# Kernel optimization log

Hardware: AMD Instinct MI355X
Metric: run time of the kernel (lower is better)

The kernel has to match this reference:

```python
import jax, jax.numpy as jnp
import numpy as np

B, N, HD = 4, 2048, 256
E, T = 4096, 1024
PROPAG_STEPS = 5
ALPHA_MAX = 0.2
LN_EPS = 1e-5


def setup_inputs() -> dict:
    key = jax.random.key(0)
    ks = jax.random.split(key, 16)
    s_in, s_h = (2.0 * HD) ** -0.5, HD ** -0.5
    return {
        "attr_matrix": jax.random.normal(ks[0], (B, N, 1), dtype=jnp.float32),
        "adj_matrix": jax.random.uniform(ks[1], (B, N, N), dtype=jnp.float32),
        # ggnn.linear_i: 1 -> HD
        "W_i": jax.random.normal(ks[2], (HD, 1), dtype=jnp.float32),
        "b_i": jnp.zeros((HD,), dtype=jnp.float32),
        # ggnn.gru: GRUCell(input=2*HD, hidden=HD), torch gate order r,z,n
        "W_ih": jax.random.normal(ks[3], (3 * HD, 2 * HD), dtype=jnp.float32) * s_in,
        "b_ih": jnp.zeros((3 * HD,), dtype=jnp.float32),
        "W_hh": jax.random.normal(ks[4], (3 * HD, HD), dtype=jnp.float32) * s_h,
        "b_hh": jnp.zeros((3 * HD,), dtype=jnp.float32),
        # ggnn.linear_o: HD -> 1
        "W_o": jax.random.normal(ks[5], (1, HD), dtype=jnp.float32) * s_h,
        "b_o": jnp.zeros((1,), dtype=jnp.float32),
        # topo buffers (incidence-like, kept small to mimic sparse +/-1 matrices)
        "B1": jax.random.normal(ks[6], (N, E), dtype=jnp.float32) * 0.02,
        "B2": jax.random.normal(ks[7], (E, T), dtype=jnp.float32) * 0.02,
        # topo trainables
        "proj_W": jax.random.normal(ks[8], (HD, HD), dtype=jnp.float32) * s_h,
        "ln_gamma": jnp.ones((HD,), dtype=jnp.float32),
        "ln_beta": jnp.zeros((HD,), dtype=jnp.float32),
        "alpha_raw": jnp.float32(-2.0),
    }


def _gru_cell(x, h, W_ih, b_ih, W_hh, b_hh):
    # x: [B,N,2H], h: [B,N,H]; torch GRUCell gate order: r, z, n
    gx = jnp.einsum('bni,gi->bng', x, W_ih) + b_ih
    gh = jnp.einsum('bnh,gh->bng', h, W_hh) + b_hh
    xr, xz, xn = jnp.split(gx, 3, axis=-1)
    hr, hz, hn = jnp.split(gh, 3, axis=-1)
    r = jax.nn.sigmoid(xr + hr)
    z = jax.nn.sigmoid(xz + hz)
    n = jnp.tanh(xn + r * hn)
    return (1.0 - z) * n + z * h


def _layernorm(x, gamma, beta):
    mu = jnp.mean(x, axis=-1, keepdims=True)
    var = jnp.mean(jnp.square(x - mu), axis=-1, keepdims=True)
    return (x - mu) * jax.lax.rsqrt(var + LN_EPS) * gamma + beta


def reference(attr_matrix, adj_matrix, W_i, b_i, W_ih, b_ih, W_hh, b_hh,
              W_o, b_o, B1, B2, proj_W, ln_gamma, ln_beta, alpha_raw):
    A_in = adj_matrix                      # [B,N,N]
    A_out = jnp.swapaxes(adj_matrix, -2, -1)
    # linear_i + relu
    h = jax.nn.relu(jnp.einsum('bnc,hc->bnh', attr_matrix, W_i) + b_i)  # [B,N,H]
    # GGNN propagation
    for _ in range(PROPAG_STEPS):
        a_in = jnp.einsum('bnm,bmh->bnh', A_in, h)
        a_out = jnp.einsum('bnm,bmh->bnh', A_out, h)
        h = _gru_cell(jnp.concatenate((a_in, a_out), axis=-1), h,
                      W_ih, b_ih, W_hh, b_hh)
    # topo residual: dH = B1 (L1 (B1^T h)), L1 = B1^T B1 + B2 B2^T
    L1 = B1.T @ B1 + B2 @ B2.T             # [E,E]
    E_feat = jnp.einsum('ne,bnh->beh', B1, h)       # B1^T H
    E_topo = jnp.einsum('ef,bfh->beh', L1, E_feat)
    dH = jnp.einsum('ne,beh->bnh', B1, E_topo)
    dH = _layernorm(jax.nn.relu(jnp.einsum('bnh,oh->bno', dH, proj_W)),
                    ln_gamma, ln_beta)
    alpha = ALPHA_MAX * jax.nn.sigmoid(alpha_raw)
    h = h + alpha * dH
    # linear_o -> [B,N] (squeeze(0) is a no-op for B>1)
    anomaly = (jnp.einsum('bnh,oh->bno', h, W_o) + b_o)[..., 0]
    return anomaly
```

## Files before the change

### kernel.cpp

```cpp
#include <hip/hip_runtime.h>
#include <hip/hip_fp16.h>


typedef __bf16 bf16x8 __attribute__((ext_vector_type(8)));
typedef _Float16 f16x8 __attribute__((ext_vector_type(8)));
typedef float f32x4 __attribute__((ext_vector_type(4)));

#define BM 128
#define BN 128
#define BK 16
#define LO_INV (1.f / 1024.f)

__device__ __forceinline__ unsigned short bf16rne(float x)
{
    unsigned u = __float_as_uint(x);
    return (unsigned short)((u + 0x7FFFu + ((u >> 16) & 1u)) >> 16);
}
__device__ __forceinline__ float bf2f(unsigned short h)
{
    return __uint_as_float((unsigned)h << 16);
}
__device__ __forceinline__ void split2(float x, unsigned short& hi, unsigned short& lo)
{
    hi = bf16rne(x);
    lo = bf16rne(x - bf2f(hi));
}

__device__ __forceinline__ unsigned short f16r(float x)
{
    return __half_as_ushort(__float2half(x));
}
__device__ __forceinline__ float f16f(unsigned short u)
{
    return __half2float(__ushort_as_half(u));
}
__device__ __forceinline__ void splitf(float x, unsigned short& hi, unsigned short& lo)
{
    hi = f16r(x);
    lo = f16r((x - f16f(hi)) * 1024.f);
}

__device__ __forceinline__ void gload_lds16(const unsigned short* g, unsigned short* l)
{
    __builtin_amdgcn_global_load_lds(
        (const __attribute__((address_space(1))) void*)g,
        (__attribute__((address_space(3))) void*)l, 16, 0, 0);
}

__device__ __forceinline__ void stage2(const unsigned short* g, unsigned short* l, int K)
{
    gload_lds16(g, l);
    gload_lds16(g + (size_t)32 * K, l + 2048);
}

template<int SPLIT>
__device__ __forceinline__ void mm_loop64f(
    const unsigned short* ag0, const unsigned short* ag1,
    const unsigned short* bg0, const unsigned short* bg1,
    int K, unsigned short* LDS, int tid,
    f32x4 (&acc0)[2][2], f32x4 (&acc1)[2][2])
{
    constexpr int NT = SPLIT ? 2 : 1;
    constexpr int TSZ = 4096;

    int lane = tid & 63, r16 = lane & 15, g = lane >> 4, s7 = r16 & 7;
    int wv = tid >> 6, wr = wv >> 1, wc = wv & 1;
    int arow = (wr * 32 + r16) * 128;
    int brow = (wc * 32 + r16) * 128;
    unsigned short* lA = LDS + (tid >> 6) * 512;
    unsigned short* lB = LDS + NT * TSZ + (tid >> 6) * 512;
    const char* Ab = (const char*)LDS;
    const char* Bb = (const char*)(LDS + NT * TSZ);

    for (int k0 = 0; k0 < K; k0 += 64) {
        stage2(ag0 + k0, lA, K);
        if constexpr (SPLIT) stage2(ag1 + k0, lA + TSZ, K);
        stage2(bg0 + k0, lB, K);
        if constexpr (SPLIT) stage2(bg1 + k0, lB + TSZ, K);
        __syncthreads();
#pragma unroll
        for (int ks = 0; ks < 2; ++ks) {
            int tt = ((ks * 4 + g) ^ s7) * 16;
            f16x8 a0[2], a1[2], b0[2], b1[2];
#pragma unroll
            for (int mi = 0; mi < 2; ++mi) {
                a0[mi] = *(const f16x8*)(Ab + arow + mi * 2048 + tt);
                if constexpr (SPLIT)
                    a1[mi] = *(const f16x8*)(Ab + TSZ * 2 + arow + mi * 2048 + tt);
            }
#pragma unroll
            for (int ni = 0; ni < 2; ++ni) {
                b0[ni] = *(const f16x8*)(Bb + brow + ni * 2048 + tt);
                if constexpr (SPLIT)
                    b1[ni] = *(const f16x8*)(Bb + TSZ * 2 + brow + ni * 2048 + tt);
            }
#pragma unroll
            for (int mi = 0; mi < 2; ++mi)
#pragma unroll
                for (int ni = 0; ni < 2; ++ni) {
                    if constexpr (SPLIT) {
                        acc1[mi][ni] = __builtin_amdgcn_mfma_f32_16x16x32_f16(
                            a1[mi], b0[ni], acc1[mi][ni], 0, 0, 0);
                        acc1[mi][ni] = __builtin_amdgcn_mfma_f32_16x16x32_f16(
                            a0[mi], b1[ni], acc1[mi][ni], 0, 0, 0);
                    }
                    acc0[mi][ni] = __builtin_amdgcn_mfma_f32_16x16x32_f16(
                        a0[mi], b0[ni], acc0[mi][ni], 0, 0, 0);
                }
        }
        __syncthreads();
    }
}

template<int SPLIT, int OF16>
__global__ __launch_bounds__(256, 2) void mm_f16(
    const unsigned short* __restrict__ Ah, const unsigned short* __restrict__ Al,
    const unsigned short* __restrict__ Bh, const unsigned short* __restrict__ Bl,
    int K, const float* __restrict__ bias, const float* __restrict__ Cacc,
    void* __restrict__ Cout, int ldc)
{
    constexpr int NT = SPLIT ? 2 : 1;
    __shared__ unsigned short LDS[2 * NT * 4096];
    int tid = threadIdx.x;

    unsigned nwg = gridDim.x * gridDim.y;
    unsigned lin = blockIdx.y * gridDim.x + blockIdx.x;
    unsigned wk = ((nwg & 7) == 0) ? (lin & 7) * (nwg >> 3) + (lin >> 3) : lin;
    unsigned bx = wk % gridDim.x, by = wk / gridDim.x;

    int m0 = by * 64, n0 = bx * 64;
    int rp = tid >> 3, sl8 = ((tid & 7) ^ (rp & 7)) * 8;
    const unsigned short* ag0 = Ah + (size_t)(m0 + rp) * K + sl8;
    const unsigned short* ag1 = SPLIT ? Al + (size_t)(m0 + rp) * K + sl8 : nullptr;
    const unsigned short* bg0 = Bh + (size_t)(n0 + rp) * K + sl8;
    const unsigned short* bg1 = SPLIT ? Bl + (size_t)(n0 + rp) * K + sl8 : nullptr;

    f32x4 acc0[2][2], acc1[2][2];
#pragma unroll
    for (int mi = 0; mi < 2; ++mi)
#pragma unroll
        for (int ni = 0; ni < 2; ++ni) {
            acc0[mi][ni] = (f32x4){0.f, 0.f, 0.f, 0.f};
            acc1[mi][ni] = (f32x4){0.f, 0.f, 0.f, 0.f};
        }

    mm_loop64f<SPLIT>(ag0, ag1, bg0, bg1, K, LDS, tid, acc0, acc1);

    int lane = tid & 63, r16 = lane & 15, g = lane >> 4;
    int wv = tid >> 6, wr = wv >> 1, wc = wv & 1;
#pragma unroll
    for (int mi = 0; mi < 2; ++mi) {
#pragma unroll
        for (int ni = 0; ni < 2; ++ni) {
            int col = n0 + wc * 32 + ni * 16 + r16;
            float badd = bias ? bias[col] : 0.f;
#pragma unroll
            for (int j = 0; j < 4; ++j) {
                int row = m0 + wr * 32 + mi * 16 + g * 4 + j;
                float v = acc0[mi][ni][j] + badd;
                if (SPLIT) v += acc1[mi][ni][j] * LO_INV;
                if (Cacc) v += Cacc[(size_t)row * ldc + col];
                if (OF16)
                    ((unsigned short*)Cout)[(size_t)row * ldc + col] = f16r(v);
                else
                    ((float*)Cout)[(size_t)row * ldc + col] = v;
            }
        }
    }
}

__global__ __launch_bounds__(256, 2) void gxgru(
    const unsigned short* __restrict__ Xhi, const unsigned short* __restrict__ Xlo,
    const unsigned short* __restrict__ WihH, const unsigned short* __restrict__ WihL,
    const float* __restrict__ b_ih, const float* __restrict__ ghb,
    float* __restrict__ h)
{
    __shared__ unsigned short LDS[32768];
    int tid = threadIdx.x;

    unsigned lin = blockIdx.y * 4 + blockIdx.x;
    unsigned wk = (lin & 7) * 64 + (lin >> 3);
    unsigned tb = wk & 3, by = wk >> 2;

    int m0 = by * 64;
    const int K = 512;
    int rp = tid >> 3, sl8 = ((tid & 7) ^ (rp & 7)) * 8;
    const unsigned short* ag0 = Xhi + (size_t)(m0 + rp) * K + sl8;
    const unsigned short* ag1 = Xlo + (size_t)(m0 + rp) * K + sl8;
    const unsigned short* bh0 = WihH + (size_t)(tb * 192 + rp) * K + sl8;
    const unsigned short* bl0 = WihL + (size_t)(tb * 192 + rp) * K + sl8;

    int lane = tid & 63, r16 = lane & 15, lg = lane >> 4, s7 = r16 & 7;
    int wv = tid >> 6, wr = wv >> 1, wc = wv & 1;
    int arow = (wr * 32 + r16) * 128;
    int brow = (wc * 32 + r16) * 128;
    unsigned short* lA = LDS + (tid >> 6) * 512;
    unsigned short* lB = LDS + 8192 + (tid >> 6) * 512;

    f32x4 acc0[3][2][2], acc1[3][2][2];
#pragma unroll
    for (int g = 0; g < 3; ++g)
#pragma unroll
        for (int mi = 0; mi < 2; ++mi)
#pragma unroll
            for (int ni = 0; ni < 2; ++ni) {
                acc0[g][mi][ni] = (f32x4){0.f, 0.f, 0.f, 0.f};
                acc1[g][mi][ni] = (f32x4){0.f, 0.f, 0.f, 0.f};
            }

    for (int k0 = 0; k0 < K; k0 += 64) {
        stage2(ag0 + k0, lA, K);
        stage2(ag1 + k0, lA + 4096, K);
#pragma unroll
        for (int g = 0; g < 3; ++g) {
            stage2(bh0 + (size_t)(g * 64) * K + k0, lB + g * 4096, K);
            stage2(bl0 + (size_t)(g * 64) * K + k0, lB + 12288 + g * 4096, K);
        }
        __syncthreads();
#pragma unroll
        for (int ks = 0; ks < 2; ++ks) {
            int tt = ((ks * 4 + lg) ^ s7) * 16;
            f16x8 a0[2], a1[2];
#pragma unroll
            for (int mi = 0; mi < 2; ++mi) {
                a0[mi] = *(const f16x8*)((const char*)LDS + arow + mi * 2048 + tt);
                a1[mi] = *(const f16x8*)((const char*)LDS + 8192 + arow + mi * 2048 + tt);
            }
#pragma unroll
            for (int g = 0; g < 3; ++g) {
                f16x8 b0[2], b1[2];
#pragma unroll
                for (int ni = 0; ni < 2; ++ni) {
                    b0[ni] = *(const f16x8*)((const char*)LDS + 16384 + g * 8192 +
                                             brow + ni * 2048 + tt);
                    b1[ni] = *(const f16x8*)((const char*)LDS + 40960 + g * 8192 +
                                             brow + ni * 2048 + tt);
                }
#pragma unroll
                for (int mi = 0; mi < 2; ++mi)
#pragma unroll
                    for (int ni = 0; ni < 2; ++ni) {
                        acc1[g][mi][ni] = __builtin_amdgcn_mfma_f32_16x16x32_f16(
                            a1[mi], b0[ni], acc1[g][mi][ni], 0, 0, 0);
                        acc1[g][mi][ni] = __builtin_amdgcn_mfma_f32_16x16x32_f16(
                            a0[mi], b1[ni], acc1[g][mi][ni], 0, 0, 0);
                        acc0[g][mi][ni] = __builtin_amdgcn_mfma_f32_16x16x32_f16(
                            a0[mi], b0[ni], acc0[g][mi][ni], 0, 0, 0);
                    }
            }
        }
        __syncthreads();
    }

#pragma unroll
    for (int mi = 0; mi < 2; ++mi) {
#pragma unroll
        for (int ni = 0; ni < 2; ++ni) {
            int t = tb * 64 + wc * 32 + ni * 16 + r16;
            float br = b_ih[t], bz = b_ih[256 + t], bn = b_ih[512 + t];
#pragma unroll
            for (int j = 0; j < 4; ++j) {
                int row = m0 + wr * 32 + mi * 16 + lg * 4 + j;
                float xr = acc0[0][mi][ni][j] + acc1[0][mi][ni][j] * LO_INV + br;
                float xz = acc0[1][mi][ni][j] + acc1[1][mi][ni][j] * LO_INV + bz;
                float xn = acc0[2][mi][ni][j] + acc1[2][mi][ni][j] * LO_INV + bn;
                size_t grow = (size_t)row * 768;
                float hr = ghb[grow + t];
                float hz = ghb[grow + 256 + t];
                float hn = ghb[grow + 512 + t];
                float r = 1.f / (1.f + __expf(-(xr + hr)));
                float z = 1.f / (1.f + __expf(-(xz + hz)));
                float nn = tanhf(xn + r * hn);
                size_t hix = (size_t)row * 256 + t;
                h[hix] = (1.f - z) * nn + z * h[hix];
            }
        }
    }
}

__global__ __launch_bounds__(256, 2) void mm_step1f(
    const unsigned short* __restrict__ AhHi, const unsigned short* __restrict__ AhLo,
    const unsigned short* __restrict__ AtHi, const unsigned short* __restrict__ AtLo,
    const unsigned short* __restrict__ hTh, const unsigned short* __restrict__ hTl,
    unsigned short* __restrict__ Xhi, unsigned short* __restrict__ Xlo,
    const unsigned short* __restrict__ hrmh, const unsigned short* __restrict__ hrml,
    const unsigned short* __restrict__ WhhH, const unsigned short* __restrict__ WhhL,
    const float* __restrict__ b_hh, float* __restrict__ ghb)
{
    __shared__ unsigned short LDS[16384];
    int tid = threadIdx.x;
    unsigned bid = blockIdx.x;
    int lane = tid & 63, r16 = lane & 15, g = lane >> 4;
    int wv = tid >> 6, wr = wv >> 1, wc = wv & 1;
    int rp = tid >> 3, sl8 = ((tid & 7) ^ (rp & 7)) * 8;

    f32x4 acc0[2][2], acc1[2][2];
#pragma unroll
    for (int mi = 0; mi < 2; ++mi)
#pragma unroll
        for (int ni = 0; ni < 2; ++ni) {
            acc0[mi][ni] = (f32x4){0.f, 0.f, 0.f, 0.f};
            acc1[mi][ni] = (f32x4){0.f, 0.f, 0.f, 0.f};
        }

    if (bid < 1024) {
        unsigned wk = (bid & 7) * 128 + (bid >> 3);
        unsigned bz = wk >> 7, rem = wk & 127, by = rem >> 2, bx = rem & 3;
        int b = bz >> 1, wio = bz & 1;
        const unsigned short* Ahp = (wio ? AtHi : AhHi) + (size_t)b * 4194304;
        const unsigned short* Alp = (wio ? AtLo : AhLo) + (size_t)b * 4194304;
        size_t boff = (size_t)(b * 256 + bx * 64) * 2048;
        int m0 = by * 64;
        const int K = 2048;
        const unsigned short* ag0 = Ahp + (size_t)(m0 + rp) * K + sl8;
        const unsigned short* ag1 = Alp + (size_t)(m0 + rp) * K + sl8;
        const unsigned short* bg0 = hTh + boff + (size_t)rp * K + sl8;
        const unsigned short* bg1 = hTl + boff + (size_t)rp * K + sl8;

        mm_loop64f<1>(ag0, ag1, bg0, bg1, K, LDS, tid, acc0, acc1);

        float* T = reinterpret_cast<float*>(LDS);
#pragma unroll
        for (int mi = 0; mi < 2; ++mi)
#pragma unroll
            for (int ni = 0; ni < 2; ++ni)
#pragma unroll
                for (int j = 0; j < 4; ++j)
                    T[(wr * 32 + mi * 16 + g * 4 + j) * 68 +
                      wc * 32 + ni * 16 + r16] =
                        acc0[mi][ni][j] + acc1[mi][ni][j] * LO_INV;
        __syncthreads();

        int row = tid >> 2, fq = tid & 3;
        const float* src = T + row * 68 + fq * 16;
        unsigned hw[8], lw[8];
#pragma unroll
        for (int e = 0; e < 8; ++e) {
            unsigned short h0, l0, h1, l1;
            splitf(src[2 * e], h0, l0);
            splitf(src[2 * e + 1], h1, l1);
            hw[e] = (unsigned)h0 | ((unsigned)h1 << 16);
            lw[e] = (unsigned)l0 | ((unsigned)l1 << 16);
        }
        size_t base = ((size_t)(m0 + row) * 4 + b) * 512 + wio * 256 + bx * 64 + fq * 16;
        ((uint4*)(Xhi + base))[0] = (uint4){hw[0], hw[1], hw[2], hw[3]};
        ((uint4*)(Xhi + base))[1] = (uint4){hw[4], hw[5], hw[6], hw[7]};
        ((uint4*)(Xlo + base))[0] = (uint4){lw[0], lw[1], lw[2], lw[3]};
        ((uint4*)(Xlo + base))[1] = (uint4){lw[4], lw[5], lw[6], lw[7]};
    } else {
        unsigned gidx = bid - 1024;
        unsigned by = gidx / 12, bx = gidx % 12;
        int m0 = by * 64, n0 = bx * 64;
        const int K = 256;
        const unsigned short* ag0 = hrmh + (size_t)(m0 + rp) * K + sl8;
        const unsigned short* ag1 = hrml + (size_t)(m0 + rp) * K + sl8;
        const unsigned short* bg0 = WhhH + (size_t)(n0 + rp) * K + sl8;
        const unsigned short* bg1 = WhhL + (size_t)(n0 + rp) * K + sl8;

        mm_loop64f<1>(ag0, ag1, bg0, bg1, K, LDS, tid, acc0, acc1);

#pragma unroll
        for (int mi = 0; mi < 2; ++mi) {
#pragma unroll
            for (int ni = 0; ni < 2; ++ni) {
                int col = n0 + wc * 32 + ni * 16 + r16;
                float badd = b_hh[col];
#pragma unroll
                for (int j = 0; j < 4; ++j) {
                    int row = m0 + wr * 32 + mi * 16 + g * 4 + j;
                    ghb[(size_t)row * 768 + col] =
                        acc0[mi][ni][j] + acc1[mi][ni][j] * LO_INV + badd;
                }
            }
        }
    }
}

__global__ void split_adj16(const float* __restrict__ adj,
                            unsigned short* __restrict__ nhi, unsigned short* __restrict__ nlo,
                            unsigned short* __restrict__ thi, unsigned short* __restrict__ tlo)
{
    __shared__ float t[64][68];
    int z = blockIdx.z;
    const float* src = adj + (size_t)z * 4194304;
    int tx = threadIdx.x & 15, ty = threadIdx.x >> 4;
    int i0 = blockIdx.y * 64, j0 = blockIdx.x * 64;
#pragma unroll
    for (int i = 0; i < 4; ++i) {
        int r = ty * 4 + i;
        float4 v = *(const float4*)(src + (size_t)(i0 + r) * 2048 + j0 + tx * 4);
        ushort4 h, l;
        splitf(v.x, h.x, l.x); splitf(v.y, h.y, l.y);
        splitf(v.z, h.z, l.z); splitf(v.w, h.w, l.w);
        size_t o = (size_t)z * 4194304 + (size_t)(i0 + r) * 2048 + j0 + tx * 4;
        *(ushort4*)(nhi + o) = h; *(ushort4*)(nlo + o) = l;
        t[r][tx * 4 + 0] = v.x; t[r][tx * 4 + 1] = v.y;
        t[r][tx * 4 + 2] = v.z; t[r][tx * 4 + 3] = v.w;
    }
    __syncthreads();
#pragma unroll
    for (int i = 0; i < 4; ++i) {
        int r = ty * 4 + i;
        ushort4 h, l;
        splitf(t[tx * 4 + 0][r], h.x, l.x);
        splitf(t[tx * 4 + 1][r], h.y, l.y);
        splitf(t[tx * 4 + 2][r], h.z, l.z);
        splitf(t[tx * 4 + 3][r], h.w, l.w);
        size_t o = (size_t)z * 4194304 + (size_t)(j0 + r) * 2048 + i0 + tx * 4;
        *(ushort4*)(thi + o) = h; *(ushort4*)(tlo + o) = l;
    }
}

__global__ void split_h16(const float* __restrict__ h,
                          unsigned short* __restrict__ hi, unsigned short* __restrict__ lo,
                          unsigned short* __restrict__ hrmh, unsigned short* __restrict__ hrml)
{
    __shared__ float t[64][68];
    int f0 = blockIdx.x * 64, n0 = blockIdx.y * 64;
    int tx = threadIdx.x & 15, ty = threadIdx.x >> 4;
#pragma unroll
    for (int i = 0; i < 4; ++i) {
        int r = ty * 4 + i;
        float4 v = *(const float4*)(h + (size_t)(n0 + r) * 1024 + f0 + tx * 4);
        t[r][tx * 4 + 0] = v.x; t[r][tx * 4 + 1] = v.y;
        t[r][tx * 4 + 2] = v.z; t[r][tx * 4 + 3] = v.w;
        if (hrmh) {
            ushort4 hh, ll;
            splitf(v.x, hh.x, ll.x); splitf(v.y, hh.y, ll.y);
            splitf(v.z, hh.z, ll.z); splitf(v.w, hh.w, ll.w);
            size_t o = (size_t)(n0 + r) * 1024 + f0 + tx * 4;
            *(ushort4*)(hrmh + o) = hh;
            *(ushort4*)(hrml + o) = ll;
        }
    }
    __syncthreads();
#pragma unroll
    for (int i = 0; i < 4; ++i) {
        int r = ty * 4 + i;
        ushort4 hh, ll;
        splitf(t[tx * 4 + 0][r], hh.x, ll.x);
        splitf(t[tx * 4 + 1][r], hh.y, ll.y);
        splitf(t[tx * 4 + 2][r], hh.z, ll.z);
        splitf(t[tx * 4 + 3][r], hh.w, ll.w);
        size_t o = (size_t)(f0 + r) * 2048 + n0 + tx * 4;
        *(ushort4*)(hi + o) = hh; *(ushort4*)(lo + o) = ll;
    }
}

__global__ void split_t16(const float* __restrict__ in, unsigned short* __restrict__ outN,
                          unsigned short* __restrict__ outT, int R, int C)
{
    __shared__ float t[64][68];
    int i0 = blockIdx.y * 64, j0 = blockIdx.x * 64;
    int tx = threadIdx.x & 15, ty = threadIdx.x >> 4;
#pragma unroll
    for (int i = 0; i < 4; ++i) {
        int r = ty * 4 + i;
        float4 v = *(const float4*)(in + (size_t)(i0 + r) * C + j0 + tx * 4);
        ushort4 hh;
        hh.x = f16r(v.x); hh.y = f16r(v.y);
        hh.z = f16r(v.z); hh.w = f16r(v.w);
        *(ushort4*)(outN + (size_t)(i0 + r) * C + j0 + tx * 4) = hh;
        t[r][tx * 4 + 0] = v.x; t[r][tx * 4 + 1] = v.y;
        t[r][tx * 4 + 2] = v.z; t[r][tx * 4 + 3] = v.w;
    }
    __syncthreads();
#pragma unroll
    for (int i = 0; i < 4; ++i) {
        int r = ty * 4 + i;
        ushort4 hh;
        hh.x = f16r(t[tx * 4 + 0][r]);
        hh.y = f16r(t[tx * 4 + 1][r]);
        hh.z = f16r(t[tx * 4 + 2][r]);
        hh.w = f16r(t[tx * 4 + 3][r]);
        *(ushort4*)(outT + (size_t)(j0 + r) * R + i0 + tx * 4) = hh;
    }
}

__global__ void split_w16(const float* __restrict__ Wih, const float* __restrict__ Whh,
                          const float* __restrict__ pj,
                          unsigned short* __restrict__ WihH, unsigned short* __restrict__ WihL,
                          unsigned short* __restrict__ WhhH, unsigned short* __restrict__ WhhL,
                          unsigned short* __restrict__ pjH)
{
    int i = blockIdx.x * 256 + threadIdx.x;
    if (i < 393216) {
        int row = i >> 9, col = i & 511;
        int g = row >> 8, t = row & 255;
        int nrow = (t >> 6) * 192 + g * 64 + (t & 63);
        unsigned short h, l;
        splitf(Wih[i], h, l);
        WihH[nrow * 512 + col] = h; WihL[nrow * 512 + col] = l;
    } else if (i < 589824) {
        int j = i - 393216;
        unsigned short h, l;
        splitf(Whh[j], h, l);
        WhhH[j] = h; WhhL[j] = l;
    } else if (i < 655360) {
        int j = i - 589824;
        pjH[j] = f16r(pj[j]);
    }
}

__global__ __launch_bounds__(256, 2) void gemm_f32(
    const float* __restrict__ A, const float* __restrict__ B, float* __restrict__ C,
    int M, int N, int K, int lda, int ldb, int ldc,
    long sA, long sB, long sC,
    const float* __restrict__ bias, int ta, int tb, int accum)
{
    int bz = blockIdx.z;
    int taEff = ta;
    if (ta == 2) {
        int b = bz >> 1, w = bz & 1;
        A += (long)b * sA; B += (long)b * sB; C += (long)b * sC + w * 256;
        taEff = w;
    } else {
        A += (long)bz * sA; B += (long)bz * sB; C += (long)bz * sC;
    }
    int m0 = blockIdx.y * BM, n0 = blockIdx.x * BN;

    __shared__ float As[BK][BM + 4];
    __shared__ float Bs[BK][BN + 4];

    int tid = threadIdx.x;
    int tx = tid & 15, ty = tid >> 4;

    float acc[64];
#pragma unroll
    for (int i = 0; i < 64; ++i) acc[i] = 0.f;

    for (int k0 = 0; k0 < K; k0 += BK) {
        if (!taEff) {
            int m = tid >> 1, kk = (tid & 1) * 8;
            const float* src = A + (long)(m0 + m) * lda + (k0 + kk);
            float4 v0 = *(const float4*)(src);
            float4 v1 = *(const float4*)(src + 4);
            As[kk + 0][m] = v0.x; As[kk + 1][m] = v0.y;
            As[kk + 2][m] = v0.z; As[kk + 3][m] = v0.w;
            As[kk + 4][m] = v1.x; As[kk + 5][m] = v1.y;
            As[kk + 6][m] = v1.z; As[kk + 7][m] = v1.w;
        } else {
            int k = tid >> 4, mm = (tid & 15) * 8;
            const float* src = A + (long)(k0 + k) * lda + (m0 + mm);
            *(float4*)&As[k][mm]     = *(const float4*)(src);
            *(float4*)&As[k][mm + 4] = *(const float4*)(src + 4);
        }
        if (!tb) {
            int k = tid >> 4, nn = (tid & 15) * 8;
            const float* src = B + (long)(k0 + k) * ldb + (n0 + nn);
            *(float4*)&Bs[k][nn]     = *(const float4*)(src);
            *(float4*)&Bs[k][nn + 4] = *(const float4*)(src + 4);
        } else {
            int n = tid >> 1, kk = (tid & 1) * 8;
            const float* src = B + (long)(n0 + n) * ldb + (k0 + kk);
            float4 v0 = *(const float4*)(src);
            float4 v1 = *(const float4*)(src + 4);
            Bs[kk + 0][n] = v0.x; Bs[kk + 1][n] = v0.y;
            Bs[kk + 2][n] = v0.z; Bs[kk + 3][n] = v0.w;
            Bs[kk + 4][n] = v1.x; Bs[kk + 5][n] = v1.y;
            Bs[kk + 6][n] = v1.z; Bs[kk + 7][n] = v1.w;
        }
        __syncthreads();

#pragma unroll
        for (int k = 0; k < BK; ++k) {
            float a[8], b[8];
            *(float4*)&a[0] = *(const float4*)&As[k][ty * 4];
            *(float4*)&a[4] = *(const float4*)&As[k][64 + ty * 4];
            *(float4*)&b[0] = *(const float4*)&Bs[k][tx * 4];
            *(float4*)&b[4] = *(const float4*)&Bs[k][64 + tx * 4];
#pragma unroll
            for (int i = 0; i < 8; ++i)
#pragma unroll
                for (int j = 0; j < 8; ++j)
                    acc[i * 8 + j] += a[i] * b[j];
        }
        __syncthreads();
    }

#pragma unroll
    for (int i = 0; i < 8; ++i) {
        int row = m0 + ((i >> 2) ? 64 : 0) + ty * 4 + (i & 3);
#pragma unroll
        for (int jh = 0; jh < 2; ++jh) {
            int col = n0 + jh * 64 + tx * 4;
            float4 v;
            v.x = acc[i * 8 + jh * 4 + 0];
            v.y = acc[i * 8 + jh * 4 + 1];
            v.z = acc[i * 8 + jh * 4 + 2];
            v.w = acc[i * 8 + jh * 4 + 3];
            if (bias) {
                v.x += bias[col + 0]; v.y += bias[col + 1];
                v.z += bias[col + 2]; v.w += bias[col + 3];
            }
            float* dst = C + (long)row * ldc + col;
            if (accum) {
                float4 o = *(const float4*)dst;
                v.x += o.x; v.y += o.y; v.z += o.z; v.w += o.w;
            }
            *(float4*)dst = v;
        }
    }
}

__global__ void split_adj(const float* __restrict__ adj,
                          unsigned short* __restrict__ nhi, unsigned short* __restrict__ nlo,
                          unsigned short* __restrict__ thi, unsigned short* __restrict__ tlo)
{
    __shared__ float t[64][68];
    int z = blockIdx.z;
    const float* src = adj + (size_t)z * 4194304;
    int tx = threadIdx.x & 15, ty = threadIdx.x >> 4;
    int i0 = blockIdx.y * 64, j0 = blockIdx.x * 64;
#pragma unroll
    for (int i = 0; i < 4; ++i) {
        int r = ty * 4 + i;
        float4 v = *(const float4*)(src + (size_t)(i0 + r) * 2048 + j0 + tx * 4);
        ushort4 h, l;
        split2(v.x, h.x, l.x); split2(v.y, h.y, l.y);
        split2(v.z, h.z, l.z); split2(v.w, h.w, l.w);
        size_t o = (size_t)z * 4194304 + (size_t)(i0 + r) * 2048 + j0 + tx * 4;
        *(ushort4*)(nhi + o) = h; *(ushort4*)(nlo + o) = l;
        t[r][tx * 4 + 0] = v.x; t[r][tx * 4 + 1] = v.y;
        t[r][tx * 4 + 2] = v.z; t[r][tx * 4 + 3] = v.w;
    }
    __syncthreads();
#pragma unroll
    for (int i = 0; i < 4; ++i) {
        int r = ty * 4 + i;
        ushort4 h, l;
        split2(t[tx * 4 + 0][r], h.x, l.x);
        split2(t[tx * 4 + 1][r], h.y, l.y);
        split2(t[tx * 4 + 2][r], h.z, l.z);
        split2(t[tx * 4 + 3][r], h.w, l.w);
        size_t o = (size_t)z * 4194304 + (size_t)(j0 + r) * 2048 + i0 + tx * 4;
        *(ushort4*)(thi + o) = h; *(ushort4*)(tlo + o) = l;
    }
}

__global__ void split_h(const float* __restrict__ h,
                        unsigned short* __restrict__ hi, unsigned short* __restrict__ lo)
{
    __shared__ float t[64][68];
    int f0 = blockIdx.x * 64, n0 = blockIdx.y * 64;
    int tx = threadIdx.x & 15, ty = threadIdx.x >> 4;
#pragma unroll
    for (int i = 0; i < 4; ++i) {
        int r = ty * 4 + i;
        float4 v = *(const float4*)(h + (size_t)(n0 + r) * 1024 + f0 + tx * 4);
        t[r][tx * 4 + 0] = v.x; t[r][tx * 4 + 1] = v.y;
        t[r][tx * 4 + 2] = v.z; t[r][tx * 4 + 3] = v.w;
    }
    __syncthreads();
#pragma unroll
    for (int i = 0; i < 4; ++i) {
        int r = ty * 4 + i;
        ushort4 hh, ll;
        split2(t[tx * 4 + 0][r], hh.x, ll.x);
        split2(t[tx * 4 + 1][r], hh.y, ll.y);
        split2(t[tx * 4 + 2][r], hh.z, ll.z);
        split2(t[tx * 4 + 3][r], hh.w, ll.w);
        size_t o = (size_t)(f0 + r) * 2048 + n0 + tx * 4;
        *(ushort4*)(hi + o) = hh; *(ushort4*)(lo + o) = ll;
    }
}

__global__ __launch_bounds__(256, 3) void adj_mfma(
    const unsigned short* __restrict__ AhHi, const unsigned short* __restrict__ AhLo,
    const unsigned short* __restrict__ AtHi, const unsigned short* __restrict__ AtLo,
    const unsigned short* __restrict__ hTHi, const unsigned short* __restrict__ hTLo,
    float* __restrict__ c0, float* __restrict__ c1, float* __restrict__ c2)
{
    __shared__ unsigned short As[8192];
    __shared__ unsigned short Bs[8192];
    int tid = threadIdx.x;
    int bz = blockIdx.z;
    int region = bz >> 3, bw = bz & 7, b = bw >> 1, w = bw & 1;
    const unsigned short* Abase =
        (region == 2) ? (w ? AtLo : AhLo) : (w ? AtHi : AhHi);
    Abase += (size_t)b * 4194304;
    const unsigned short* Bbase = (region == 1) ? hTLo : hTHi;
    float* Cb = (region == 0) ? c0 : (region == 1 ? c1 : c2);

    int m0 = blockIdx.y * 128;
    int f0 = b * 256 + blockIdx.x * 128;

    int rp = tid >> 3;
    int sl = (tid & 7) ^ (rp & 7);
    const unsigned short* ag = Abase + (size_t)(m0 + rp) * 2048 + sl * 8;
    const unsigned short* bg = Bbase + (size_t)(f0 + rp) * 2048 + sl * 8;
    unsigned short* al = &As[(tid >> 6) * 512];
    unsigned short* bl = &Bs[(tid >> 6) * 512];

    int lane = tid & 63, r16 = lane & 15, g = lane >> 4;
    int wv = tid >> 6, wr = wv >> 1, wc = wv & 1;
    int s7 = r16 & 7;
    int t0 = (g ^ s7) * 16, t1 = ((4 + g) ^ s7) * 16;
    int arow = (wr * 64 + r16) * 128;
    int brow = (wc * 64 + r16) * 128;

    f32x4 acc[4][4];
#pragma unroll
    for (int mi = 0; mi < 4; ++mi)
#pragma unroll
        for (int ni = 0; ni < 4; ++ni)
            acc[mi][ni] = (f32x4){0.f, 0.f, 0.f, 0.f};

    for (int k0 = 0; k0 < 2048; k0 += 64) {
#pragma unroll
        for (int i = 0; i < 4; ++i)
            gload_lds16(ag + k0 + (size_t)i * 65536, al + i * 2048);
#pragma unroll
        for (int i = 0; i < 4; ++i)
            gload_lds16(bg + k0 + (size_t)i * 65536, bl + i * 2048);
        __syncthreads();

#pragma unroll
        for (int ks = 0; ks < 2; ++ks) {
            int tt = ks ? t1 : t0;
            bf16x8 af[4], bf[4];
#pragma unroll
            for (int mi = 0; mi < 4; ++mi)
                af[mi] = *(const bf16x8*)((const char*)As + arow + mi * 2048 + tt);
#pragma unroll
            for (int ni = 0; ni < 4; ++ni)
                bf[ni] = *(const bf16x8*)((const char*)Bs + brow + ni * 2048 + tt);
#pragma unroll
            for (int mi = 0; mi < 4; ++mi)
#pragma unroll
                for (int ni = 0; ni < 4; ++ni)
                    acc[mi][ni] = __builtin_amdgcn_mfma_f32_16x16x32_bf16(
                        af[mi], bf[ni], acc[mi][ni], 0, 0, 0);
        }
        __syncthreads();
    }

    int cbase = b * 512 + w * 256 + blockIdx.x * 128 + wc * 64;
#pragma unroll
    for (int mi = 0; mi < 4; ++mi) {
        int row = m0 + wr * 64 + mi * 16 + g * 4;
#pragma unroll
        for (int ni = 0; ni < 4; ++ni) {
            int col = cbase + ni * 16 + r16;
            float* dst = Cb + (size_t)row * 2048 + col;
#pragma unroll
            for (int j = 0; j < 4; ++j) dst[(size_t)j * 2048] = acc[mi][ni][j];
        }
    }
}

__global__ void reduce3(float4* __restrict__ x, const float4* __restrict__ p,
                        const float4* __restrict__ q)
{
    int i = blockIdx.x * 256 + threadIdx.x;
    float4 a = x[i], b = p[i], c = q[i];
    a.x += b.x + c.x; a.y += b.y + c.y; a.z += b.z + c.z; a.w += b.w + c.w;
    x[i] = a;
}

__global__ void init_h(const float* __restrict__ attr, const float* __restrict__ W_i,
                       const float* __restrict__ b_i, float* __restrict__ h)
{
    int n = blockIdx.x, b = blockIdx.y, t = threadIdx.x;
    float a = attr[b * 2048 + n];
    h[(long)n * 1024 + b * 256 + t] = fmaxf(a * W_i[t] + b_i[t], 0.f);
}

__global__ void gru_ew(const float* __restrict__ gx, const float* __restrict__ gh,
                       float* __restrict__ h)
{
    int n = blockIdx.x, b = blockIdx.y, t = threadIdx.x;
    long row = ((long)n * 4 + b) * 768;
    float xr = gx[row + t], xz = gx[row + 256 + t], xn = gx[row + 512 + t];
    float hr = gh[row + t], hz = gh[row + 256 + t], hn = gh[row + 512 + t];
    float r = 1.f / (1.f + __expf(-(xr + hr)));
    float z = 1.f / (1.f + __expf(-(xz + hz)));
    float nn = tanhf(xn + r * hn);
    long hi = (long)n * 1024 + b * 256 + t;
    float ho = h[hi];
    h[hi] = (1.f - z) * nn + z * ho;
}

__global__ void ln_out(const float* __restrict__ dP, const float* __restrict__ gamma,
                       const float* __restrict__ beta, const float* __restrict__ araw,
                       const float* __restrict__ h, const float* __restrict__ W_o,
                       const float* __restrict__ b_o, float* __restrict__ out)
{
    int n = blockIdx.x, b = blockIdx.y, t = threadIdx.x;
    long row = ((long)n * 4 + b) * 256;
    float v = fmaxf(dP[row + t], 0.f);
    float s = v, s2 = v * v;
#pragma unroll
    for (int o = 1; o < 64; o <<= 1) { s += __shfl_xor(s, o); s2 += __shfl_xor(s2, o); }
    __shared__ float red[8];
    int w = t >> 6, lane = t & 63;
    if (lane == 0) { red[w] = s; red[4 + w] = s2; }
    __syncthreads();
    float S  = red[0] + red[1] + red[2] + red[3];
    float S2 = red[4] + red[5] + red[6] + red[7];
    float mu = S * (1.f / 256.f);
    float var = S2 * (1.f / 256.f) - mu * mu;
    float rs = rsqrtf(var + 1e-5f);
    float alpha = 0.2f / (1.f + __expf(-araw[0]));
    float y = h[(long)n * 1024 + b * 256 + t] +
              alpha * ((v - mu) * rs * gamma[t] + beta[t]);
    float d = y * W_o[t];
#pragma unroll
    for (int o = 1; o < 64; o <<= 1) d += __shfl_xor(d, o);
    __syncthreads();
    if (lane == 0) red[w] = d;
    __syncthreads();
    if (t == 0) out[(long)b * 2048 + n] = red[0] + red[1] + red[2] + red[3] + b_o[0];
}

__global__ void ln_residual(const float* __restrict__ dP, const float* __restrict__ gamma,
                            const float* __restrict__ beta, const float* __restrict__ araw,
                            float* __restrict__ h)
{
    int n = blockIdx.x, b = blockIdx.y, t = threadIdx.x;
    long row = ((long)n * 4 + b) * 256;
    float v = fmaxf(dP[row + t], 0.f);
    float s = v, s2 = v * v;
#pragma unroll
    for (int o = 1; o < 64; o <<= 1) { s += __shfl_xor(s, o); s2 += __shfl_xor(s2, o); }
    __shared__ float red[8];
    int w = t >> 6, lane = t & 63;
    if (lane == 0) { red[w] = s; red[4 + w] = s2; }
    __syncthreads();
    float S  = red[0] + red[1] + red[2] + red[3];
    float S2 = red[4] + red[5] + red[6] + red[7];
    float mu = S * (1.f / 256.f);
    float var = S2 * (1.f / 256.f) - mu * mu;
    float rs = rsqrtf(var + 1e-5f);
    float alpha = 0.2f / (1.f + __expf(-araw[0]));
    long hi = (long)n * 1024 + b * 256 + t;
    h[hi] += alpha * ((v - mu) * rs * gamma[t] + beta[t]);
}

__global__ void out_kernel(const float* __restrict__ h, const float* __restrict__ W_o,
                           const float* __restrict__ b_o, float* __restrict__ out)
{
    int t = threadIdx.x;
    int w = t >> 6, lane = t & 63;
    int row = blockIdx.x * 4 + w;
    int n = row >> 2, b = row & 3;
    const float* hp = h + (long)n * 1024 + b * 256;
    float s = 0.f;
#pragma unroll
    for (int i = 0; i < 4; ++i) { int c = i * 64 + lane; s += hp[c] * W_o[c]; }
#pragma unroll
    for (int o = 1; o < 64; o <<= 1) s += __shfl_xor(s, o);
    if (lane == 0) out[(long)b * 2048 + n] = s + b_o[0];
}

extern "C" void kernel_launch(void* const* d_in, const int* in_sizes, int n_in,
                              void* d_out, int out_size, void* d_ws, size_t ws_size,
                              hipStream_t stream)
{
    (void)in_sizes; (void)n_in; (void)out_size;
    const float* attr  = (const float*)d_in[0];
    const float* adj   = (const float*)d_in[1];
    const float* W_i   = (const float*)d_in[2];
    const float* b_i   = (const float*)d_in[3];
    const float* W_ih  = (const float*)d_in[4];
    const float* b_ih  = (const float*)d_in[5];
    const float* W_hh  = (const float*)d_in[6];
    const float* b_hh  = (const float*)d_in[7];
    const float* W_o   = (const float*)d_in[8];
    const float* b_o   = (const float*)d_in[9];
    const float* B1    = (const float*)d_in[10];
    const float* B2    = (const float*)d_in[11];
    const float* projW = (const float*)d_in[12];
    const float* gamma = (const float*)d_in[13];
    const float* beta  = (const float*)d_in[14];
    const float* araw  = (const float*)d_in[15];
    float* out = (float*)d_out;

    char* wsb = (char*)d_ws;
    dim3 blk(256);

    const size_t REQ1 = 0xD400000;
    const size_t REQ2 = 0xD000000;

    if (ws_size >= REQ1) {
        float* hbuf = (float*)(wsb);
        float* gxb  = (float*)(wsb + 0x0800000);
        unsigned short* hrmh = (unsigned short*)(wsb + 0x0800000);
        unsigned short* hrml = (unsigned short*)(wsb + 0x0C00000);
        unsigned short* hTh  = (unsigned short*)(wsb + 0x1800000);
        unsigned short* hTl  = (unsigned short*)(wsb + 0x1C00000);
        float* ghb  = (float*)(wsb + 0x2000000);
        unsigned short* Xhi = (unsigned short*)(wsb + 0x3800000);
        unsigned short* Xlo = (unsigned short*)(wsb + 0x4000000);
        unsigned short* Wih_h = (unsigned short*)(wsb + 0x5000000);
        unsigned short* Wih_l = (unsigned short*)(wsb + 0x50C0000);
        unsigned short* Whh_h = (unsigned short*)(wsb + 0x5240000);
        unsigned short* Whh_l = (unsigned short*)(wsb + 0x52A0000);
        unsigned short* pjh   = (unsigned short*)(wsb + 0x5300000);
        char* R1 = wsb + 0x5400000;
        unsigned short* AhHi = (unsigned short*)(R1);
        unsigned short* AhLo = (unsigned short*)(R1 + 0x2000000);
        unsigned short* AtHi = (unsigned short*)(R1 + 0x4000000);
        unsigned short* AtLo = (unsigned short*)(R1 + 0x6000000);
        unsigned short* B1h = (unsigned short*)(R1);
        unsigned short* B1T = (unsigned short*)(R1 + 0x1000000);
        unsigned short* B2h = (unsigned short*)(R1 + 0x2000000);
        unsigned short* B2T = (unsigned short*)(R1 + 0x2800000);
        unsigned short* uTb = (unsigned short*)(R1 + 0x3000000);
        unsigned short* pTb = (unsigned short*)(R1 + 0x3800000);
        unsigned short* rTb = (unsigned short*)(R1 + 0x3C00000);
        unsigned short* qTb = (unsigned short*)(R1 + 0x3E00000);
        float* qTf = gxb;
        unsigned short* dHb = (unsigned short*)(wsb + 0x1800000);
        float* dPb = ghb;

        init_h<<<dim3(2048, 4), blk, 0, stream>>>(attr, W_i, b_i, hbuf);
        split_adj16<<<dim3(32, 32, 4), blk, 0, stream>>>(adj, AhHi, AhLo, AtHi, AtLo);
        split_w16<<<dim3(2560), blk, 0, stream>>>(W_ih, W_hh, projW,
            Wih_h, Wih_l, Whh_h, Whh_l, pjh);

        for (int step = 0; step < 5; ++step) {
            split_h16<<<dim3(16, 32), blk, 0, stream>>>(hbuf, hTh, hTl, hrmh, hrml);
            mm_step1f<<<dim3(2560), blk, 0, stream>>>(
                AhHi, AhLo, AtHi, AtLo, hTh, hTl, Xhi, Xlo,
                hrmh, hrml, Whh_h, Whh_l, b_hh, ghb);
            gxgru<<<dim3(4, 128), blk, 0, stream>>>(
                Xhi, Xlo, Wih_h, Wih_l, b_ih, ghb, hbuf);
        }

        split_h16<<<dim3(16, 32), blk, 0, stream>>>(hbuf, hTh, hTl, nullptr, nullptr);
        split_t16<<<dim3(64, 32), blk, 0, stream>>>(B1, B1h, B1T, 2048, 4096);
        split_t16<<<dim3(16, 64), blk, 0, stream>>>(B2, B2h, B2T, 4096, 1024);
        mm_f16<0, 1><<<dim3(64, 16), blk, 0, stream>>>(
            hTh, nullptr, B1T, nullptr, 2048, nullptr, nullptr, uTb, 4096);
        mm_f16<0, 1><<<dim3(32, 16), blk, 0, stream>>>(
            uTb, nullptr, B1h, nullptr, 4096, nullptr, nullptr, pTb, 2048);
        mm_f16<0, 1><<<dim3(16, 16), blk, 0, stream>>>(
            uTb, nullptr, B2T, nullptr, 4096, nullptr, nullptr, rTb, 1024);
        mm_f16<0, 0><<<dim3(64, 16), blk, 0, stream>>>(
            pTb, nullptr, B1T, nullptr, 2048, nullptr, nullptr, qTf, 4096);
        mm_f16<0, 1><<<dim3(64, 16), blk, 0, stream>>>(
            rTb, nullptr, B2h, nullptr, 1024, nullptr, qTf, qTb, 4096);
        mm_f16<0, 1><<<dim3(16, 32), blk, 0, stream>>>(
            B1h, nullptr, qTb, nullptr, 4096, nullptr, nullptr, dHb, 1024);
        mm_f16<0, 0><<<dim3(4, 128), blk, 0, stream>>>(
            dHb, nullptr, pjh, nullptr, 256, nullptr, nullptr, dPb, 256);

        ln_out<<<dim3(2048, 4), blk, 0, stream>>>(dPb, gamma, beta, araw,
                                                  hbuf, W_o, b_o, out);
        return;
    }

    float* hbuf = (float*)(wsb);
    float* xbuf = (float*)(wsb + 0x800000);
    float* gxb  = (float*)(wsb + 0x1800000);
    float* ghb  = (float*)(wsb + 0x3000000);
    unsigned short* AhHi = (unsigned short*)(wsb + 0x4800000);
    unsigned short* AhLo = (unsigned short*)(wsb + 0x6800000);
    unsigned short* AtHi = (unsigned short*)(wsb + 0x8800000);
    unsigned short* AtLo = (unsigned short*)(wsb + 0xA800000);
    unsigned short* hTHi = (unsigned short*)(wsb + 0xC800000);
    unsigned short* hTLo = (unsigned short*)(wsb + 0xCC00000);

    float* ub  = xbuf;
    float* pb  = gxb;
    float* qb  = gxb + (1 << 21);
    float* rb  = ghb;
    float* dHr = ghb + (1 << 20);
    float* dPb = ghb + 3 * (1 << 20);

    bool mfma_path = (ws_size >= REQ2);

    init_h<<<dim3(2048, 4), blk, 0, stream>>>(attr, W_i, b_i, hbuf);

    if (mfma_path)
        split_adj<<<dim3(32, 32, 4), blk, 0, stream>>>(adj, AhHi, AhLo, AtHi, AtLo);

    for (int step = 0; step < 5; ++step) {
        if (mfma_path) {
            split_h<<<dim3(16, 32), blk, 0, stream>>>(hbuf, hTHi, hTLo);
            adj_mfma<<<dim3(2, 16, 24), blk, 0, stream>>>(
                AhHi, AhLo, AtHi, AtLo, hTHi, hTLo, xbuf, gxb, ghb);
            reduce3<<<dim3(4096), blk, 0, stream>>>(
                (float4*)xbuf, (const float4*)gxb, (const float4*)ghb);
        } else {
            gemm_f32<<<dim3(2, 16, 8), blk, 0, stream>>>(
                adj, hbuf, xbuf, 2048, 256, 2048, 2048, 1024, 2048,
                (long)2048 * 2048, 256, 512, nullptr, 2, 0, 0);
        }
        gemm_f32<<<dim3(6, 64, 1), blk, 0, stream>>>(
            xbuf, W_ih, gxb, 8192, 768, 512, 512, 512, 768,
            0, 0, 0, b_ih, 0, 1, 0);
        gemm_f32<<<dim3(6, 64, 1), blk, 0, stream>>>(
            hbuf, W_hh, ghb, 8192, 768, 256, 256, 256, 768,
            0, 0, 0, b_hh, 0, 1, 0);
        gru_ew<<<dim3(2048, 4), blk, 0, stream>>>(gxb, ghb, hbuf);
    }

    gemm_f32<<<dim3(8, 32, 1), blk, 0, stream>>>(
        B1, hbuf, ub, 4096, 1024, 2048, 4096, 1024, 1024, 0, 0, 0, nullptr, 1, 0, 0);
    gemm_f32<<<dim3(8, 16, 1), blk, 0, stream>>>(
        B1, ub, pb, 2048, 1024, 4096, 4096, 1024, 1024, 0, 0, 0, nullptr, 0, 0, 0);
    gemm_f32<<<dim3(8, 32, 1), blk, 0, stream>>>(
        B1, pb, qb, 4096, 1024, 2048, 4096, 1024, 1024, 0, 0, 0, nullptr, 1, 0, 0);
    gemm_f32<<<dim3(8, 8, 1), blk, 0, stream>>>(
        B2, ub, rb, 1024, 1024, 4096, 1024, 1024, 1024, 0, 0, 0, nullptr, 1, 0, 0);
    gemm_f32<<<dim3(8, 32, 1), blk, 0, stream>>>(
        B2, rb, qb, 4096, 1024, 1024, 1024, 1024, 1024, 0, 0, 0, nullptr, 0, 0, 1);
    gemm_f32<<<dim3(8, 16, 1), blk, 0, stream>>>(
        B1, qb, dHr, 2048, 1024, 4096, 4096, 1024, 1024, 0, 0, 0, nullptr, 0, 0, 0);
    gemm_f32<<<dim3(2, 64, 1), blk, 0, stream>>>(
        dHr, projW, dPb, 8192, 256, 256, 256, 256, 256, 0, 0, 0, nullptr, 0, 1, 0);

    ln_residual<<<dim3(2048, 4), blk, 0, stream>>>(dPb, gamma, beta, araw, hbuf);
    out_kernel<<<dim3(2048), blk, 0, stream>>>(hbuf, W_o, b_o, out);
}
```

Before: 780.9 us.

## Fuse h split into GRU epilogue and concatenate B1/B2 topo GEMMs

The GRU gate kernel now stages the updated h tile in LDS and writes the fp16 hi/lo row-major and transposed copies directly. This removes the per-step split_h16 launch and its extra read of h. The topo chain adds leading-dimension parameters to the GEMM kernel and lays B1^T and B2 side by side in one concatenated buffer. Two separate GEMMs plus an fp32 intermediate accumulate become a single K=3072 GEMM. In exchange, the GRU epilogue does more work and needs an extra LDS barrier.

```diff
diff --git a/kernel.cpp b/kernel.cpp
--- a/kernel.cpp
+++ b/kernel.cpp
@@ -47,17 +47,17 @@
         (__attribute__((address_space(3))) void*)l, 16, 0, 0);
 }
 
-__device__ __forceinline__ void stage2(const unsigned short* g, unsigned short* l, int K)
+__device__ __forceinline__ void stage2(const unsigned short* g, unsigned short* l, int ld)
 {
     gload_lds16(g, l);
-    gload_lds16(g + (size_t)32 * K, l + 2048);
+    gload_lds16(g + (size_t)32 * ld, l + 2048);
 }
 
 template<int SPLIT>
 __device__ __forceinline__ void mm_loop64f(
     const unsigned short* ag0, const unsigned short* ag1,
     const unsigned short* bg0, const unsigned short* bg1,
-    int K, unsigned short* LDS, int tid,
+    int K, int lda, int ldb, unsigned short* LDS, int tid,
     f32x4 (&acc0)[2][2], f32x4 (&acc1)[2][2])
 {
     constexpr int NT = SPLIT ? 2 : 1;
@@ -73,10 +73,10 @@
     const char* Bb = (const char*)(LDS + NT * TSZ);
 
     for (int k0 = 0; k0 < K; k0 += 64) {
-        stage2(ag0 + k0, lA, K);
-        if constexpr (SPLIT) stage2(ag1 + k0, lA + TSZ, K);
-        stage2(bg0 + k0, lB, K);
-        if constexpr (SPLIT) stage2(bg1 + k0, lB + TSZ, K);
+        stage2(ag0 + k0, lA, lda);
+        if constexpr (SPLIT) stage2(ag1 + k0, lA + TSZ, lda);
+        stage2(bg0 + k0, lB, ldb);
+        if constexpr (SPLIT) stage2(bg1 + k0, lB + TSZ, ldb);
         __syncthreads();
 #pragma unroll
         for (int ks = 0; ks < 2; ++ks) {
@@ -115,7 +115,9 @@
 template<int SPLIT, int OF16>
 __global__ __launch_bounds__(256, 2) void mm_f16(
     const unsigned short* __restrict__ Ah, const unsigned short* __restrict__ Al,
+    int lda,
     const unsigned short* __restrict__ Bh, const unsigned short* __restrict__ Bl,
+    int ldb,
     int K, const float* __restrict__ bias, const float* __restrict__ Cacc,
     void* __restrict__ Cout, int ldc)
 {
@@ -130,10 +132,10 @@
 
     int m0 = by * 64, n0 = bx * 64;
     int rp = tid >> 3, sl8 = ((tid & 7) ^ (rp & 7)) * 8;
-    const unsigned short* ag0 = Ah + (size_t)(m0 + rp) * K + sl8;
-    const unsigned short* ag1 = SPLIT ? Al + (size_t)(m0 + rp) * K + sl8 : nullptr;
-    const unsigned short* bg0 = Bh + (size_t)(n0 + rp) * K + sl8;
-    const unsigned short* bg1 = SPLIT ? Bl + (size_t)(n0 + rp) * K + sl8 : nullptr;
+    const unsigned short* ag0 = Ah + (size_t)(m0 + rp) * lda + sl8;
+    const unsigned short* ag1 = SPLIT ? Al + (size_t)(m0 + rp) * lda + sl8 : nullptr;
+    const unsigned short* bg0 = Bh + (size_t)(n0 + rp) * ldb + sl8;
+    const unsigned short* bg1 = SPLIT ? Bl + (size_t)(n0 + rp) * ldb + sl8 : nullptr;
 
     f32x4 acc0[2][2], acc1[2][2];
 #pragma unroll
@@ -144,7 +146,7 @@
             acc1[mi][ni] = (f32x4){0.f, 0.f, 0.f, 0.f};
         }
 
-    mm_loop64f<SPLIT>(ag0, ag1, bg0, bg1, K, LDS, tid, acc0, acc1);
+    mm_loop64f<SPLIT>(ag0, ag1, bg0, bg1, K, lda, ldb, LDS, tid, acc0, acc1);
 
     int lane = tid & 63, r16 = lane & 15, g = lane >> 4;
     int wv = tid >> 6, wr = wv >> 1, wc = wv & 1;
@@ -173,7 +175,9 @@
     const unsigned short* __restrict__ Xhi, const unsigned short* __restrict__ Xlo,
     const unsigned short* __restrict__ WihH, const unsigned short* __restrict__ WihL,
     const float* __restrict__ b_ih, const float* __restrict__ ghb,
-    float* __restrict__ h)
+    float* __restrict__ h,
+    unsigned short* __restrict__ hrmh, unsigned short* __restrict__ hrml,
+    unsigned short* __restrict__ hTh, unsigned short* __restrict__ hTl)
 {
     __shared__ unsigned short LDS[32768];
     int tid = threadIdx.x;
@@ -252,15 +256,18 @@
         __syncthreads();
     }
 
+    float* T2 = reinterpret_cast<float*>(LDS);
 #pragma unroll
     for (int mi = 0; mi < 2; ++mi) {
 #pragma unroll
         for (int ni = 0; ni < 2; ++ni) {
-            int t = tb * 64 + wc * 32 + ni * 16 + r16;
+            int tl = wc * 32 + ni * 16 + r16;
+            int t = tb * 64 + tl;
             float br = b_ih[t], bz = b_ih[256 + t], bn = b_ih[512 + t];
 #pragma unroll
             for (int j = 0; j < 4; ++j) {
-                int row = m0 + wr * 32 + mi * 16 + lg * 4 + j;
+                int rl = wr * 32 + mi * 16 + lg * 4 + j;
+                int row = m0 + rl;
                 float xr = acc0[0][mi][ni][j] + acc1[0][mi][ni][j] * LO_INV + br;
                 float xz = acc0[1][mi][ni][j] + acc1[1][mi][ni][j] * LO_INV + bz;
                 float xn = acc0[2][mi][ni][j] + acc1[2][mi][ni][j] * LO_INV + bn;
@@ -272,9 +279,57 @@
                 float z = 1.f / (1.f + __expf(-(xz + hz)));
                 float nn = tanhf(xn + r * hn);
                 size_t hix = (size_t)row * 256 + t;
-                h[hix] = (1.f - z) * nn + z * h[hix];
+                T2[rl * 64 + tl] = (1.f - z) * nn + z * h[hix];
             }
         }
+    }
+    __syncthreads();
+
+    {
+        int rl = tid >> 2, tq = tid & 3;
+        const float* src = T2 + rl * 64 + tq * 16;
+        int row = m0 + rl;
+        int tbase = tb * 64 + tq * 16;
+        unsigned hw[8], lw[8];
+#pragma unroll
+        for (int e = 0; e < 8; ++e) {
+            unsigned short h0, l0, h1, l1;
+            splitf(src[2 * e], h0, l0);
+            splitf(src[2 * e + 1], h1, l1);
+            hw[e] = (unsigned)h0 | ((unsigned)h1 << 16);
+            lw[e] = (unsigned)l0 | ((unsigned)l1 << 16);
+        }
+        float* hd = h + (size_t)row * 256 + tbase;
+#pragma unroll
+        for (int q = 0; q < 4; ++q)
+            ((float4*)hd)[q] = *(const float4*)(src + q * 4);
+        size_t ro = (size_t)row * 256 + tbase;
+        ((uint4*)(hrmh + ro))[0] = (uint4){hw[0], hw[1], hw[2], hw[3]};
+        ((uint4*)(hrmh + ro))[1] = (uint4){hw[4], hw[5], hw[6], hw[7]};
+        ((uint4*)(hrml + ro))[0] = (uint4){lw[0], lw[1], lw[2], lw[3]};
+        ((uint4*)(hrml + ro))[1] = (uint4){lw[4], lw[5], lw[6], lw[7]};
+    }
+
+    {
+        int b = tid >> 6, tl = tid & 63;
+        int f = b * 256 + tb * 64 + tl;
+        int nbase = m0 >> 2;
+        unsigned hw[8], lw[8];
+#pragma unroll
+        for (int e = 0; e < 8; ++e) {
+            float x0 = T2[(4 * (2 * e) + b) * 64 + tl];
+            float x1 = T2[(4 * (2 * e + 1) + b) * 64 + tl];
+            unsigned short h0, l0, h1, l1;
+            splitf(x0, h0, l0);
+            splitf(x1, h1, l1);
+            hw[e] = (unsigned)h0 | ((unsigned)h1 << 16);
+            lw[e] = (unsigned)l0 | ((unsigned)l1 << 16);
+        }
+        size_t fo = (size_t)f * 2048 + nbase;
+        ((uint4*)(hTh + fo))[0] = (uint4){hw[0], hw[1], hw[2], hw[3]};
+        ((uint4*)(hTh + fo))[1] = (uint4){hw[4], hw[5], hw[6], hw[7]};
+        ((uint4*)(hTl + fo))[0] = (uint4){lw[0], lw[1], lw[2], lw[3]};
+        ((uint4*)(hTl + fo))[1] = (uint4){lw[4], lw[5], lw[6], lw[7]};
     }
 }
 
@@ -317,7 +372,7 @@
         const unsigned short* bg0 = hTh + boff + (size_t)rp * K + sl8;
         const unsigned short* bg1 = hTl + boff + (size_t)rp * K + sl8;
 
-        mm_loop64f<1>(ag0, ag1, bg0, bg1, K, LDS, tid, acc0, acc1);
+        mm_loop64f<1>(ag0, ag1, bg0, bg1, K, K, K, LDS, tid, acc0, acc1);
 
         float* T = reinterpret_cast<float*>(LDS);
 #pragma unroll
@@ -357,7 +412,7 @@
         const unsigned short* bg0 = WhhH + (size_t)(n0 + rp) * K + sl8;
         const unsigned short* bg1 = WhhL + (size_t)(n0 + rp) * K + sl8;
 
-        mm_loop64f<1>(ag0, ag1, bg0, bg1, K, LDS, tid, acc0, acc1);
+        mm_loop64f<1>(ag0, ag1, bg0, bg1, K, K, K, LDS, tid, acc0, acc1);
 
 #pragma unroll
         for (int mi = 0; mi < 2; ++mi) {
@@ -447,8 +502,10 @@
     }
 }
 
-__global__ void split_t16(const float* __restrict__ in, unsigned short* __restrict__ outN,
-                          unsigned short* __restrict__ outT, int R, int C)
+__global__ void split_t16(const float* __restrict__ in,
+                          unsigned short* __restrict__ outN, int ldN,
+                          unsigned short* __restrict__ outT, int ldT,
+                          int R, int C)
 {
     __shared__ float t[64][68];
     int i0 = blockIdx.y * 64, j0 = blockIdx.x * 64;
@@ -460,7 +517,7 @@
         ushort4 hh;
         hh.x = f16r(v.x); hh.y = f16r(v.y);
         hh.z = f16r(v.z); hh.w = f16r(v.w);
-        *(ushort4*)(outN + (size_t)(i0 + r) * C + j0 + tx * 4) = hh;
+        *(ushort4*)(outN + (size_t)(i0 + r) * ldN + j0 + tx * 4) = hh;
         t[r][tx * 4 + 0] = v.x; t[r][tx * 4 + 1] = v.y;
         t[r][tx * 4 + 2] = v.z; t[r][tx * 4 + 3] = v.w;
     }
@@ -473,7 +530,7 @@
         hh.y = f16r(t[tx * 4 + 1][r]);
         hh.z = f16r(t[tx * 4 + 2][r]);
         hh.w = f16r(t[tx * 4 + 3][r]);
-        *(ushort4*)(outT + (size_t)(j0 + r) * R + i0 + tx * 4) = hh;
+        *(ushort4*)(outT + (size_t)(j0 + r) * ldT + i0 + tx * 4) = hh;
     }
 }
 
@@ -884,7 +941,6 @@
 
     if (ws_size >= REQ1) {
         float* hbuf = (float*)(wsb);
-        float* gxb  = (float*)(wsb + 0x0800000);
         unsigned short* hrmh = (unsigned short*)(wsb + 0x0800000);
         unsigned short* hrml = (unsigned short*)(wsb + 0x0C00000);
         unsigned short* hTh  = (unsigned short*)(wsb + 0x1800000);
@@ -902,49 +958,52 @@
         unsigned short* AhLo = (unsigned short*)(R1 + 0x2000000);
         unsigned short* AtHi = (unsigned short*)(R1 + 0x4000000);
         unsigned short* AtLo = (unsigned short*)(R1 + 0x6000000);
-        unsigned short* B1h = (unsigned short*)(R1);
-        unsigned short* B1T = (unsigned short*)(R1 + 0x1000000);
-        unsigned short* B2h = (unsigned short*)(R1 + 0x2000000);
-        unsigned short* B2T = (unsigned short*)(R1 + 0x2800000);
-        unsigned short* uTb = (unsigned short*)(R1 + 0x3000000);
-        unsigned short* pTb = (unsigned short*)(R1 + 0x3800000);
-        unsigned short* rTb = (unsigned short*)(R1 + 0x3C00000);
-        unsigned short* qTb = (unsigned short*)(R1 + 0x3E00000);
-        float* qTf = gxb;
-        unsigned short* dHb = (unsigned short*)(wsb + 0x1800000);
+        unsigned short* B1h  = (unsigned short*)(R1);
+        unsigned short* B2T  = (unsigned short*)(R1 + 0x1000000);
+        unsigned short* uTb  = (unsigned short*)(R1 + 0x1800000);
+        unsigned short* prT  = (unsigned short*)(R1 + 0x2000000);
+        unsigned short* qTb  = (unsigned short*)(R1 + 0x2600000);
+        unsigned short* Bcat = (unsigned short*)(R1 + 0x2E00000);
+        unsigned short* dHb  = (unsigned short*)(wsb + 0x1800000);
         float* dPb = ghb;
 
         init_h<<<dim3(2048, 4), blk, 0, stream>>>(attr, W_i, b_i, hbuf);
         split_adj16<<<dim3(32, 32, 4), blk, 0, stream>>>(adj, AhHi, AhLo, AtHi, AtLo);
         split_w16<<<dim3(2560), blk, 0, stream>>>(W_ih, W_hh, projW,
             Wih_h, Wih_l, Whh_h, Whh_l, pjh);
+        split_h16<<<dim3(16, 32), blk, 0, stream>>>(hbuf, hTh, hTl, hrmh, hrml);
 
         for (int step = 0; step < 5; ++step) {
-            split_h16<<<dim3(16, 32), blk, 0, stream>>>(hbuf, hTh, hTl, hrmh, hrml);
             mm_step1f<<<dim3(2560), blk, 0, stream>>>(
                 AhHi, AhLo, AtHi, AtLo, hTh, hTl, Xhi, Xlo,
                 hrmh, hrml, Whh_h, Whh_l, b_hh, ghb);
             gxgru<<<dim3(4, 128), blk, 0, stream>>>(
-                Xhi, Xlo, Wih_h, Wih_l, b_ih, ghb, hbuf);
-        }
-
-        split_h16<<<dim3(16, 32), blk, 0, stream>>>(hbuf, hTh, hTl, nullptr, nullptr);
-        split_t16<<<dim3(64, 32), blk, 0, stream>>>(B1, B1h, B1T, 2048, 4096);
-        split_t16<<<dim3(16, 64), blk, 0, stream>>>(B2, B2h, B2T, 4096, 1024);
+                Xhi, Xlo, Wih_h, Wih_l, b_ih, ghb, hbuf,
+                hrmh, hrml, hTh, hTl);
+        }
+
+        split_t16<<<dim3(64, 32), blk, 0, stream>>>(B1, B1h, 4096, Bcat, 3072,
+                                                    2048, 4096);
+        split_t16<<<dim3(16, 64), blk, 0, stream>>>(B2, Bcat + 2048, 3072, B2T, 4096,
+                                                    4096, 1024);
         mm_f16<0, 1><<<dim3(64, 16), blk, 0, stream>>>(
-            hTh, nullptr, B1T, nullptr, 2048, nullptr, nullptr, uTb, 4096);
+            hTh, nullptr, 2048, Bcat, nullptr, 3072,
+            2048, nullptr, nullptr, uTb, 4096);
         mm_f16<0, 1><<<dim3(32, 16), blk, 0, stream>>>(
-            uTb, nullptr, B1h, nullptr, 4096, nullptr, nullptr, pTb, 2048);
+            uTb, nullptr, 4096, B1h, nullptr, 4096,
+            4096, nullptr, nullptr, prT, 3072);
         mm_f16<0, 1><<<dim3(16, 16), blk, 0, stream>>>(
-            uTb, nullptr, B2T, nullptr, 4096, nullptr, nullptr, rTb, 1024);
-        mm_f16<0, 0><<<dim3(64, 16), blk, 0, stream>>>(
-            pTb, nullptr, B1T, nullptr, 2048, nullptr, nullptr, qTf, 4096);
+            uTb, nullptr, 4096, B2T, nullptr, 4096,
+            4096, nullptr, nullptr, prT + 2048, 3072);
         mm_f16<0, 1><<<dim3(64, 16), blk, 0, stream>>>(
-            rTb, nullptr, B2h, nullptr, 1024, nullptr, qTf, qTb, 4096);
+            prT, nullptr, 3072, Bcat, nullptr, 3072,
+            3072, nullptr, nullptr, qTb, 4096);
         mm_f16<0, 1><<<dim3(16, 32), blk, 0, stream>>>(
-            B1h, nullptr, qTb, nullptr, 4096, nullptr, nullptr, dHb, 1024);
+            B1h, nullptr, 4096, qTb, nullptr, 4096,
+            4096, nullptr, nullptr, dHb, 1024);
         mm_f16<0, 0><<<dim3(4, 128), blk, 0, stream>>>(
-            dHb, nullptr, pjh, nullptr, 256, nullptr, nullptr, dPb, 256);
+            dHb, nullptr, 256, pjh, nullptr, 256,
+            256, nullptr, nullptr, dPb, 256);
 
         ln_out<<<dim3(2048, 4), blk, 0, stream>>>(dPb, gamma, beta, araw,
                                                   hbuf, W_o, b_o, out);
```

New measurement: 785.7 us. About the same (+0.6%).
